# Kernel optimization log

Hardware: AMD Instinct MI355X
Metric: run time of the kernel (lower is better)

The kernel has to match this reference:

```python
import jax, jax.numpy as jnp
import numpy as np

N_NODES = 50000
N_EDGES = 800000
IN_DIM = 128
HID = 64
HEADS = 4
EMB = 128
N_GRAPHS = 64
NEG_SLOPE = 0.2


def setup_inputs() -> dict:
    key = jax.random.key(0)
    ks = jax.random.split(key, 12)
    x = jax.random.normal(ks[0], (N_NODES, IN_DIM), dtype=jnp.float32)
    edge_index = jax.random.randint(ks[1], (2, N_EDGES), 0, N_NODES, dtype=jnp.int64)
    edge_weight = jax.random.uniform(ks[2], (N_EDGES,), dtype=jnp.float32)
    batch_vec = jnp.sort(jax.random.randint(ks[3], (N_NODES,), 0, N_GRAPHS, dtype=jnp.int64))
    # GATConv layer 1: in_dim -> hid, heads=4, concat
    s1 = 1.0 / np.sqrt(IN_DIM)
    W1 = jax.random.uniform(ks[4], (IN_DIM, HEADS * HID), jnp.float32, -s1, s1)
    a_src1 = jax.random.uniform(ks[5], (HEADS, HID), jnp.float32, -s1, s1)
    a_dst1 = jax.random.uniform(ks[6], (HEADS, HID), jnp.float32, -s1, s1)
    b1 = jnp.zeros((HEADS * HID,), jnp.float32)
    # GATConv layer 2: heads*hid -> emb, heads=1, mean
    s2 = 1.0 / np.sqrt(HEADS * HID)
    W2 = jax.random.uniform(ks[7], (HEADS * HID, EMB), jnp.float32, -s2, s2)
    a_src2 = jax.random.uniform(ks[8], (1, EMB), jnp.float32, -s2, s2)
    a_dst2 = jax.random.uniform(ks[9], (1, EMB), jnp.float32, -s2, s2)
    b2 = jnp.zeros((EMB,), jnp.float32)
    return {"x": x, "edge_index": edge_index, "edge_weight": edge_weight,
            "batch_vec": batch_vec, "W1": W1, "a_src1": a_src1, "a_dst1": a_dst1,
            "b1": b1, "W2": W2, "a_src2": a_src2, "a_dst2": a_dst2, "b2": b2}


def gat_conv(x, src, dst, W, a_src, a_dst, bias, heads, out_dim, concat):
    N = x.shape[0]
    h = (x @ W).reshape(N, heads, out_dim)                 # [N,H,C]
    alpha_s = jnp.sum(h * a_src, axis=-1)                  # [N,H]
    alpha_d = jnp.sum(h * a_dst, axis=-1)                  # [N,H]
    e = jax.nn.leaky_relu(alpha_s[src] + alpha_d[dst], NEG_SLOPE)  # [E,H]
    # segment softmax over edges grouped by destination node
    m = jax.ops.segment_max(e, dst, num_segments=N)        # [N,H]
    w = jnp.exp(e - m[dst])
    z = jax.ops.segment_sum(w, dst, num_segments=N)
    alpha = w / z[dst]                                     # [E,H]
    msg = h[src] * alpha[:, :, None]                       # [E,H,C]
    out = jax.ops.segment_sum(msg, dst, num_segments=N)    # [N,H,C]
    out = out.reshape(N, heads * out_dim) if concat else out.mean(axis=1)
    return out + bias


def reference(x, edge_index, edge_weight, batch_vec, W1, a_src1, a_dst1, b1, W2, a_src2, a_dst2, b2):
    N = x.shape[0]
    loop = jnp.arange(N, dtype=edge_index.dtype)
    src = jnp.concatenate([edge_index[0], loop])           # add_self_loops=True
    dst = jnp.concatenate([edge_index[1], loop])
    h = gat_conv(x, src, dst, W1, a_src1, a_dst1, b1, HEADS, HID, True)
    h = jax.nn.elu(h)                                      # dropout = identity (eval mode)
    h = gat_conv(h, src, dst, W2, a_src2, a_dst2, b2, 1, EMB, False)
    h = jax.nn.elu(h)
    # global mean pool over batch_vec
    sums = jax.ops.segment_sum(h, batch_vec, num_segments=N_GRAPHS)
    cnts = jax.ops.segment_sum(jnp.ones((N,), h.dtype), batch_vec, num_segments=N_GRAPHS)
    return sums / jnp.maximum(cnts, 1.0)[:, None]
```

## Files before the change

kernel.cpp:

```cpp
#include <hip/hip_runtime.h>
#include <hip/hip_bf16.h>
#include <cstddef>

constexpr int N_NODES = 50000;
constexpr int N_EDGES = 800000;
constexpr int IN_DIM  = 128;
constexpr int HID     = 64;
constexpr int HEADS   = 4;
constexpr int F1      = HEADS * HID;
constexpr int EMB     = 128;
constexpr int N_GRAPHS = 64;

constexpr int DEG_BLOCKS   = (N_EDGES + 255) / 256;
constexpr int SCAN_BLOCKS  = (N_NODES + 255) / 256;
constexpr int XCONV_BLOCKS = (N_NODES * IN_DIM / 4) / 256;
constexpr int W1_FRAG = 4 * 4 * 64 * 8;
constexpr int LDSB = 264;
constexpr int AXS  = HEADS * IN_DIM + 8;
constexpr int NBUCK    = (N_NODES + 255) / 256;
constexpr int P1_CHUNK = 8192;
constexpr int P1_BLOCKS = (N_EDGES + P1_CHUNK - 1) / P1_CHUNK;
constexpr int AS_BLOCKS = N_NODES / 16;
constexpr int AGG12_BLOCKS = N_NODES / 16;
static_assert(N_NODES % 16 == 0, "16-row tiling assumes exact fit");

typedef __bf16 bf16x8 __attribute__((ext_vector_type(8)));
typedef __bf16 bf16x2 __attribute__((ext_vector_type(2)));
typedef float  f32x4  __attribute__((ext_vector_type(4)));

__device__ __forceinline__ float lrelu(float x) { return x > 0.f ? x : 0.2f * x; }
__device__ __forceinline__ float eluf(float x)  { return x > 0.f ? x : expm1f(x); }

__device__ __forceinline__ void pack_frag(const float* __restrict__ B,
                                          __bf16* __restrict__ hi,
                                          __bf16* __restrict__ lo,
                                          int pblk, int NT, int KK, int ld, int col0) {
    const int gid = pblk * 256 + threadIdx.x;
    if (gid >= NT * KK * 64) return;
    const int lane = gid & 63;
    const int rem  = gid >> 6;
    const int kk   = rem % KK;
    const int t    = rem / KK;
    const int n    = col0 + t * 16 + (lane & 15);
    const int k0   = kk * 32 + (lane >> 4) * 8;
#pragma unroll
    for (int j = 0; j < 8; j++) {
        const float v = B[(size_t)(k0 + j) * ld + n];
        const __bf16 h = (__bf16)v;
        hi[(size_t)gid * 8 + j] = h;
        lo[(size_t)gid * 8 + j] = (__bf16)(v - (float)h);
    }
}

__global__ __launch_bounds__(256) void prep_kernel(const int* __restrict__ ei,
                                                   int* __restrict__ deg,
                                                   const float* __restrict__ W1,
                                                   __bf16* __restrict__ B1h,
                                                   __bf16* __restrict__ B1l,
                                                   const float* __restrict__ W2,
                                                   __bf16* __restrict__ B2h,
                                                   __bf16* __restrict__ B2l,
                                                   const float* __restrict__ as1v,
                                                   const float* __restrict__ ad1v,
                                                   float* __restrict__ wst,
                                                   const float* __restrict__ x,
                                                   __bf16* __restrict__ xb) {
    const int b = blockIdx.x;
    if (b < DEG_BLOCKS) {
        const int e = b * 256 + threadIdx.x;
        if (e < N_EDGES) atomicAdd(&deg[ei[N_EDGES + e]], 1);
        return;
    }
    const int pb = b - DEG_BLOCKS;
    if (pb < 16) {
        const int head = pb >> 2;
        pack_frag(W1, B1h + head * W1_FRAG, B1l + head * W1_FRAG,
                  pb & 3, 4, 4, F1, head * HID);
        return;
    }
    if (pb < 32) {
        pack_frag(W2, B2h, B2l, pb - 16, 8, 8, EMB, 0);
        return;
    }
    if (pb < 36) {
        const int gid = (pb - 32) * 256 + threadIdx.x;
        const int o = gid >> 7, c = gid & 127;
        const int h = o & 3;
        const float* av = (o < 4) ? as1v : ad1v;
        float s = 0.f;
#pragma unroll 8
        for (int k = 0; k < HID; k++)
            s += W1[(size_t)c * F1 + h * HID + k] * av[h * HID + k];
        wst[o * IN_DIM + c] = s;
        return;
    }
    const int i = (pb - 36) * 256 + threadIdx.x;
    const float4 v = *(const float4*)&x[(size_t)i * 4];
    __bf16 o[4] = {(__bf16)v.x, (__bf16)v.y, (__bf16)v.z, (__bf16)v.w};
    *(ulong1*)&xb[(size_t)i * 4] = *(ulong1*)o;
}

__global__ __launch_bounds__(256) void scanA_kernel(const int* __restrict__ deg,
                                                    int* __restrict__ off,
                                                    int* __restrict__ partial, int N) {
    __shared__ int sm[256];
    const int t = threadIdx.x;
    const int i = blockIdx.x * 256 + t;
    const int v = (i < N) ? deg[i] : 0;
    sm[t] = v;
    __syncthreads();
    int val = v;
#pragma unroll
    for (int o = 1; o < 256; o <<= 1) {
        const int add = (t >= o) ? sm[t - o] : 0;
        __syncthreads();
        val += add;
        sm[t] = val;
        __syncthreads();
    }
    if (i < N) off[i] = val - v;
    if (t == 255) partial[blockIdx.x] = val;
}

__global__ __launch_bounds__(256) void scanB_kernel(int* __restrict__ partial,
                                                    int* __restrict__ off_last) {
    __shared__ int sm[256];
    const int t = threadIdx.x;
    const int v = (t < SCAN_BLOCKS) ? partial[t] : 0;
    sm[t] = v;
    __syncthreads();
    int val = v;
#pragma unroll
    for (int o = 1; o < 256; o <<= 1) {
        const int add = (t >= o) ? sm[t - o] : 0;
        __syncthreads();
        val += add;
        sm[t] = val;
        __syncthreads();
    }
    if (t < SCAN_BLOCKS) partial[t] = val - v;
    if (t == SCAN_BLOCKS - 1) *off_last = val;
}

__global__ __launch_bounds__(256) void scanC_kernel(int* __restrict__ off,
                                                    const int* __restrict__ partial,
                                                    int* __restrict__ cur,
                                                    int* __restrict__ gcur, int N) {
    const int i = blockIdx.x * 256 + threadIdx.x;
    if (i < N) {
        const int o = off[i] + partial[blockIdx.x];
        off[i] = o;
        cur[i] = 0;
        if ((i & 255) == 0) gcur[i >> 8] = o;
    }
}

__global__ __launch_bounds__(256) void as_scatter_kernel(
        const float* __restrict__ x, const float* __restrict__ wst,
        float* __restrict__ as_out, float* __restrict__ ad_out,
        const int* __restrict__ ei, int* __restrict__ gcur,
        unsigned* __restrict__ stage) {
    const int tid = threadIdx.x;
    if (blockIdx.x < AS_BLOCKS) {
        const int n   = blockIdx.x * 16 + (tid >> 4);
        const int l16 = tid & 15;
        const int d8  = l16 * 8;
        const float4 xa = *(const float4*)&x[(size_t)n * IN_DIM + d8];
        const float4 xc = *(const float4*)&x[(size_t)n * IN_DIM + d8 + 4];
        float p[8];
#pragma unroll
        for (int o = 0; o < 8; o++) {
            const float4 wa = *(const float4*)&wst[o * IN_DIM + d8];
            const float4 wb = *(const float4*)&wst[o * IN_DIM + d8 + 4];
            p[o] = xa.x * wa.x + xa.y * wa.y + xa.z * wa.z + xa.w * wa.w
                 + xc.x * wb.x + xc.y * wb.y + xc.z * wb.z + xc.w * wb.w;
        }
#pragma unroll
        for (int off = 1; off < 16; off <<= 1) {
#pragma unroll
            for (int o = 0; o < 8; o++) p[o] += __shfl_xor(p[o], off);
        }
        if (l16 == 0) {
            *(float4*)&as_out[n * HEADS] = (float4){p[0], p[1], p[2], p[3]};
            *(float4*)&ad_out[n * HEADS] = (float4){p[4], p[5], p[6], p[7]};
        }
        return;
    }
    __shared__ int lhist[NBUCK];
    __shared__ int lbase[NBUCK];
    const int e0 = (blockIdx.x - AS_BLOCKS) * P1_CHUNK;
    for (int b = tid; b < NBUCK; b += 256) lhist[b] = 0;
    __syncthreads();
    for (int i = 0; i < P1_CHUNK / 256; i++) {
        const int e = e0 + i * 256 + tid;
        if (e < N_EDGES) atomicAdd(&lhist[ei[N_EDGES + e] >> 8], 1);
    }
    __syncthreads();
    for (int b = tid; b < NBUCK; b += 256) {
        const int c = lhist[b];
        lbase[b] = c ? atomicAdd(&gcur[b], c) : 0;
    }
    __syncthreads();
    for (int b = tid; b < NBUCK; b += 256) lhist[b] = 0;
    __syncthreads();
    for (int i = 0; i < P1_CHUNK / 256; i++) {
        const int e = e0 + i * 256 + tid;
        if (e < N_EDGES) {
            const int s = ei[e], d = ei[N_EDGES + e];
            const int bk = d >> 8;
            const int r  = atomicAdd(&lhist[bk], 1);
            stage[lbase[bk] + r] = (unsigned)s | ((unsigned)d << 16);
        }
    }
}

__global__ __launch_bounds__(256) void w1s_kernel(const unsigned* __restrict__ stage,
                                                  const int* __restrict__ off,
                                                  int* __restrict__ cur,
                                                  const float* __restrict__ as1,
                                                  const float* __restrict__ ad1,
                                                  int* __restrict__ col,
                                                  float4* __restrict__ w4, int E) {
    const int i = blockIdx.x * 256 + threadIdx.x;
    if (i >= E) return;
    const unsigned p = stage[i];
    const int s = (int)(p & 0xFFFFu);
    const int d = (int)(p >> 16);
    const float4 a = *(const float4*)&as1[s * HEADS];
    const float4 b = *(const float4*)&ad1[d * HEADS];
    const int pos = off[d] + atomicAdd(&cur[d], 1);
    float4 o;
    o.x = __expf(lrelu(a.x + b.x));
    o.y = __expf(lrelu(a.y + b.y));
    o.z = __expf(lrelu(a.z + b.z));
    o.w = __expf(lrelu(a.w + b.w));
    col[pos] = s;
    w4[pos] = o;
}

__global__ __launch_bounds__(256, 4) void agg_gemm12_kernel(
        const int* __restrict__ off, const int* __restrict__ col,
        const float4* __restrict__ w4, const __bf16* __restrict__ xb,
        const float* __restrict__ as1, const float* __restrict__ ad1,
        const __bf16* __restrict__ B1h, const __bf16* __restrict__ B1l,
        const float* __restrict__ b1,
        const __bf16* __restrict__ B2h, const __bf16* __restrict__ B2l,
        const float* __restrict__ avs, const float* __restrict__ avd,
        __bf16* __restrict__ g2b, float* __restrict__ as_out,
        float* __restrict__ ad_out, int M) {
    __shared__ __bf16 axh[16 * AXS];
    __shared__ __bf16 axl[16 * AXS];
    __shared__ float pps[4][16], pdd[4][16];
    __bf16* const smh = axh;
    __bf16* const sml = axl;
    const int tid  = threadIdx.x;
    const int wave = tid >> 6, lane = tid & 63;
    const int quad = lane >> 4, l16 = lane & 15;
    const int row0 = blockIdx.x * 16;

    {
        const int ln = wave * 4 + quad;
        const int w  = row0 + ln;
        const int d8 = l16 * 8;
        float acc[HEADS][8];
        float z[HEADS];
        {
            const float4 asv = *(const float4*)&as1[w * HEADS];
            const float4 adv = *(const float4*)&ad1[w * HEADS];
            const float ws0 = __expf(lrelu(asv.x + adv.x));
            const float ws1 = __expf(lrelu(asv.y + adv.y));
            const float ws2 = __expf(lrelu(asv.z + adv.z));
            const float ws3 = __expf(lrelu(asv.w + adv.w));
            const bf16x8 xv = *(const bf16x8*)&xb[(size_t)w * IN_DIM + d8];
#pragma unroll
            for (int d = 0; d < 8; d++) {
                const float xf = (float)xv[d];
                acc[0][d] = ws0 * xf; acc[1][d] = ws1 * xf;
                acc[2][d] = ws2 * xf; acc[3][d] = ws3 * xf;
            }
            z[0] = ws0; z[1] = ws1; z[2] = ws2; z[3] = ws3;
        }
        const int jb = off[w], je = off[w + 1];
        int j = jb;
        for (; j + 3 < je; j += 4) {
            int    s[4];
            float4 ww[4];
            bf16x8 bv[4];
#pragma unroll
            for (int u = 0; u < 4; u++) s[u] = col[j + u];
#pragma unroll
            for (int u = 0; u < 4; u++) ww[u] = w4[j + u];
#pragma unroll
            for (int u = 0; u < 4; u++)
                bv[u] = *(const bf16x8*)&xb[(size_t)s[u] * IN_DIM + d8];
#pragma unroll
            for (int u = 0; u < 4; u++) {
#pragma unroll
                for (int d = 0; d < 8; d++) {
                    const float xf = (float)bv[u][d];
                    acc[0][d] += ww[u].x * xf;
                    acc[1][d] += ww[u].y * xf;
                    acc[2][d] += ww[u].z * xf;
                    acc[3][d] += ww[u].w * xf;
                }
                z[0] += ww[u].x; z[1] += ww[u].y;
                z[2] += ww[u].z; z[3] += ww[u].w;
            }
        }
        for (; j < je; j++) {
            const int s0 = col[j];
            const float4 w0 = w4[j];
            const bf16x8 b0 = *(const bf16x8*)&xb[(size_t)s0 * IN_DIM + d8];
#pragma unroll
            for (int d = 0; d < 8; d++) {
                const float xf = (float)b0[d];
                acc[0][d] += w0.x * xf; acc[1][d] += w0.y * xf;
                acc[2][d] += w0.z * xf; acc[3][d] += w0.w * xf;
            }
            z[0] += w0.x; z[1] += w0.y; z[2] += w0.z; z[3] += w0.w;
        }
#pragma unroll
        for (int h = 0; h < HEADS; h++) {
            const float inv = 1.f / z[h];
            bf16x8 hv, lv;
#pragma unroll
            for (int d = 0; d < 8; d++) {
                const float v = acc[h][d] * inv;
                const __bf16 hh = (__bf16)v;
                hv[d] = hh;
                lv[d] = (__bf16)(v - (float)hh);
            }
            const int o = ln * AXS + h * IN_DIM + d8;
            *(bf16x8*)&axh[o] = hv;
            *(bf16x8*)&axl[o] = lv;
        }
    }
    __syncthreads();

    {
        bf16x8 ahv[4], alv[4];
        const int abase = l16 * AXS + wave * IN_DIM;
#pragma unroll
        for (int kk = 0; kk < 4; kk++) {
            const int k0 = kk * 32 + quad * 8;
            ahv[kk] = *(const bf16x8*)&axh[abase + k0];
            alv[kk] = *(const bf16x8*)&axl[abase + k0];
        }
        __syncthreads();

        f32x4 acc1[4];
#pragma unroll
        for (int t = 0; t < 4; t++) acc1[t] = (f32x4){0.f, 0.f, 0.f, 0.f};
#pragma unroll
        for (int kk = 0; kk < 4; kk++) {
#pragma unroll
            for (int t = 0; t < 4; t++) {
                const size_t bi = (size_t)wave * W1_FRAG +
                                  ((size_t)(t * 4 + kk) * 64 + lane) * 8;
                bf16x8 bhv = *(const bf16x8*)&B1h[bi];
                bf16x8 blv = *(const bf16x8*)&B1l[bi];
                acc1[t] = __builtin_amdgcn_mfma_f32_16x16x32_bf16(ahv[kk], bhv, acc1[t], 0, 0, 0);
                acc1[t] = __builtin_amdgcn_mfma_f32_16x16x32_bf16(alv[kk], bhv, acc1[t], 0, 0, 0);
                acc1[t] = __builtin_amdgcn_mfma_f32_16x16x32_bf16(ahv[kk], blv, acc1[t], 0, 0, 0);
            }
        }
#pragma unroll
        for (int t = 0; t < 4; t++) {
            const int c = wave * 64 + t * 16 + l16;
            const float bb = b1[c];
#pragma unroll
            for (int r = 0; r < 4; r++) {
                const float v = eluf(acc1[t][r] + bb);
                const __bf16 hh = (__bf16)v;
                smh[(quad * 4 + r) * LDSB + c] = hh;
                sml[(quad * 4 + r) * LDSB + c] = (__bf16)(v - (float)hh);
            }
        }
    }
    __syncthreads();

    f32x4 acc2[2];
#pragma unroll
    for (int t = 0; t < 2; t++) acc2[t] = (f32x4){0.f, 0.f, 0.f, 0.f};
    const int arow = l16 * LDSB;
#pragma unroll
    for (int kk = 0; kk < 8; kk++) {
        const int k0 = kk * 32 + quad * 8;
        bf16x8 ah = *(const bf16x8*)&smh[arow + k0];
        bf16x8 al = *(const bf16x8*)&sml[arow + k0];
#pragma unroll
        for (int tt = 0; tt < 2; tt++) {
            const int t = wave * 2 + tt;
            const size_t bi = ((size_t)(t * 8 + kk) * 64 + lane) * 8;
            bf16x8 bhv = *(const bf16x8*)&B2h[bi];
            bf16x8 blv = *(const bf16x8*)&B2l[bi];
            acc2[tt] = __builtin_amdgcn_mfma_f32_16x16x32_bf16(ah, bhv, acc2[tt], 0, 0, 0);
            acc2[tt] = __builtin_amdgcn_mfma_f32_16x16x32_bf16(al, bhv, acc2[tt], 0, 0, 0);
            acc2[tt] = __builtin_amdgcn_mfma_f32_16x16x32_bf16(ah, blv, acc2[tt], 0, 0, 0);
        }
    }

    const int rowS = row0 + quad * 4;
#pragma unroll
    for (int tt = 0; tt < 2; tt++) {
        const int t = wave * 2 + tt;
#pragma unroll
        for (int r = 0; r < 4; r++) {
            const int rr = rowS + r;
            if (rr < M) g2b[(size_t)rr * EMB + t * 16 + l16] = (__bf16)acc2[tt][r];
        }
    }
#pragma unroll
    for (int r = 0; r < 4; r++) {
        float ps = 0.f, pd = 0.f;
#pragma unroll
        for (int tt = 0; tt < 2; tt++) {
            const int c = (wave * 2 + tt) * 16 + l16;
            ps += acc2[tt][r] * avs[c];
            pd += acc2[tt][r] * avd[c];
        }
#pragma unroll
        for (int o = 1; o < 16; o <<= 1) {
            ps += __shfl_xor(ps, o);
            pd += __shfl_xor(pd, o);
        }
        if (l16 == 0) {
            pps[wave][quad * 4 + r] = ps;
            pdd[wave][quad * 4 + r] = pd;
        }
    }
    __syncthreads();
    if (tid < 16) {
        const int rr = row0 + tid;
        if (rr < M) {
            as_out[rr] = pps[0][tid] + pps[1][tid] + pps[2][tid] + pps[3][tid];
            ad_out[rr] = pdd[0][tid] + pdd[1][tid] + pdd[2][tid] + pdd[3][tid];
        }
    }
}

__global__ __launch_bounds__(256) void agg2_kernel(const int* __restrict__ off,
                                                   const int* __restrict__ col,
                                                   const float* __restrict__ as2,
                                                   const float* __restrict__ ad2,
                                                   const __bf16* __restrict__ g2b,
                                                   float* __restrict__ out2, int N) {
    const int w  = blockIdx.x * 16 + (threadIdx.x >> 4);
    const int d8 = (threadIdx.x & 15) * 8;
    const float ad2w = ad2[w];
    float acc[8];
    float z;
    {
        const float wt = __expf(lrelu(as2[w] + ad2w));
        const bf16x8 hv = *(const bf16x8*)&g2b[(size_t)w * EMB + d8];
#pragma unroll
        for (int d = 0; d < 8; d++) acc[d] = wt * (float)hv[d];
        z = wt;
    }
    const int jb = off[w], je = off[w + 1];
    int j = jb;
    for (; j + 3 < je; j += 4) {
        int s[4];
#pragma unroll
        for (int u = 0; u < 4; u++) s[u] = col[j + u];
        float av[4];
#pragma unroll
        for (int u = 0; u < 4; u++) av[u] = as2[s[u]];
        bf16x8 bv[4];
#pragma unroll
        for (int u = 0; u < 4; u++)
            bv[u] = *(const bf16x8*)&g2b[(size_t)s[u] * EMB + d8];
#pragma unroll
        for (int u = 0; u < 4; u++) {
            const float wt = __expf(lrelu(av[u] + ad2w));
#pragma unroll
            for (int d = 0; d < 8; d++) acc[d] += wt * (float)bv[u][d];
            z += wt;
        }
    }
    for (; j < je; j++) {
        const int s0 = col[j];
        const float wt = __expf(lrelu(as2[s0] + ad2w));
        const bf16x8 b0 = *(const bf16x8*)&g2b[(size_t)s0 * EMB + d8];
#pragma unroll
        for (int d = 0; d < 8; d++) acc[d] += wt * (float)b0[d];
        z += wt;
    }
    const float inv = 1.f / z;
    float4 o0, o1;
    o0.x = acc[0] * inv; o0.y = acc[1] * inv; o0.z = acc[2] * inv; o0.w = acc[3] * inv;
    o1.x = acc[4] * inv; o1.y = acc[5] * inv; o1.z = acc[6] * inv; o1.w = acc[7] * inv;
    *(float4*)&out2[(size_t)w * EMB + d8]     = o0;
    *(float4*)&out2[(size_t)w * EMB + d8 + 4] = o1;
}

__global__ __launch_bounds__(128) void pool_kernel(const float* __restrict__ out2,
                                                   const float* __restrict__ b2,
                                                   const int* __restrict__ batch,
                                                   float* __restrict__ pool,
                                                   float* __restrict__ cnt, int N) {
    const int c = threadIdx.x;
    const int n0 = blockIdx.x * 64;
    const int nend = min(n0 + 64, N);
    const float bias = b2[c];
    float acc = 0.f, cacc = 0.f;
    int curg = batch[n0];
    for (int n = n0; n < nend; n++) {
        const int g = batch[n];
        if (g != curg) {
            atomicAdd(&pool[curg * EMB + c], acc);
            if (c == 0) atomicAdd(&cnt[curg], cacc);
            acc = 0.f; cacc = 0.f; curg = g;
        }
        float v = out2[(size_t)n * EMB + c] + bias;
        v = v > 0.f ? v : expm1f(v);
        acc += v;
        cacc += 1.f;
    }
    atomicAdd(&pool[curg * EMB + c], acc);
    if (c == 0) atomicAdd(&cnt[curg], cacc);
}

__global__ __launch_bounds__(256) void div_kernel(const float* __restrict__ pool,
                                                  const float* __restrict__ cnt,
                                                  float* __restrict__ out) {
    const int i = blockIdx.x * 256 + threadIdx.x;
    out[i] = pool[i] / fmaxf(cnt[i >> 7], 1.f);
}

extern "C" void kernel_launch(void* const* d_in, const int* in_sizes, int n_in,
                              void* d_out, int out_size, void* d_ws, size_t ws_size,
                              hipStream_t stream) {
    const float* x      = (const float*)d_in[0];
    const int*   ei     = (const int*)d_in[1];
    const int*   batch  = (const int*)d_in[3];
    const float* W1     = (const float*)d_in[4];
    const float* a_src1 = (const float*)d_in[5];
    const float* a_dst1 = (const float*)d_in[6];
    const float* b1     = (const float*)d_in[7];
    const float* W2     = (const float*)d_in[8];
    const float* a_src2 = (const float*)d_in[9];
    const float* a_dst2 = (const float*)d_in[10];
    const float* b2     = (const float*)d_in[11];
    float* out = (float*)d_out;

    const int N = N_NODES, E = N_EDGES;

    size_t cur_off = 0;
    auto carve = [&](size_t bytes) {
        size_t o = cur_off;
        cur_off = (cur_off + bytes + 255) & ~(size_t)255;
        return (char*)d_ws + o;
    };
    int* deg     = (int*)carve((size_t)N * 4);
    float* pool  = (float*)carve((size_t)N_GRAPHS * EMB * 4);
    float* cnt   = (float*)carve((size_t)N_GRAPHS * 4);
    const size_t zero_bytes = cur_off;
    int* curp    = (int*)carve((size_t)N * 4);
    int* partial = (int*)carve((size_t)SCAN_BLOCKS * 4);
    int* gcur    = (int*)carve((size_t)NBUCK * 4);
    unsigned* stage = (unsigned*)carve((size_t)E * 4);
    float* wst   = (float*)carve((size_t)8 * IN_DIM * 4);
    __bf16* B1h  = (__bf16*)carve((size_t)HEADS * W1_FRAG * 2);
    __bf16* B1l  = (__bf16*)carve((size_t)HEADS * W1_FRAG * 2);
    __bf16* B2h  = (__bf16*)carve((size_t)F1 * EMB * 2);
    __bf16* B2l  = (__bf16*)carve((size_t)F1 * EMB * 2);
    __bf16* xb   = (__bf16*)carve((size_t)N * IN_DIM * 2);
    int* off     = (int*)carve((size_t)(N + 1) * 4);
    int* col     = (int*)carve((size_t)E * 4);
    float4* w4   = (float4*)carve((size_t)E * 16);
    __bf16* g2b  = (__bf16*)carve((size_t)N * EMB * 2);
    float* out2  = (float*)carve((size_t)N * EMB * 4);
    float* as1   = (float*)carve((size_t)N * HEADS * 4);
    float* ad1   = (float*)carve((size_t)N * HEADS * 4);
    float* as2   = (float*)carve((size_t)N * 4);
    float* ad2   = (float*)carve((size_t)N * 4);

    hipMemsetAsync(d_ws, 0, zero_bytes, stream);

    prep_kernel<<<DEG_BLOCKS + 36 + XCONV_BLOCKS, 256, 0, stream>>>(
        ei, deg, W1, B1h, B1l, W2, B2h, B2l, a_src1, a_dst1, wst, x, xb);

    scanA_kernel<<<SCAN_BLOCKS, 256, 0, stream>>>(deg, off, partial, N);
    scanB_kernel<<<1, 256, 0, stream>>>(partial, &off[N]);
    scanC_kernel<<<SCAN_BLOCKS, 256, 0, stream>>>(off, partial, curp, gcur, N);

    as_scatter_kernel<<<AS_BLOCKS + P1_BLOCKS, 256, 0, stream>>>(
        x, wst, as1, ad1, ei, gcur, stage);

    w1s_kernel<<<DEG_BLOCKS, 256, 0, stream>>>(stage, off, curp, as1, ad1, col, w4, E);

    agg_gemm12_kernel<<<AGG12_BLOCKS, 256, 0, stream>>>(off, col, w4, xb, as1, ad1,
                                                        B1h, B1l, b1, B2h, B2l,
                                                        a_src2, a_dst2,
                                                        g2b, as2, ad2, N);

    agg2_kernel<<<AGG12_BLOCKS, 256, 0, stream>>>(off, col, as2, ad2, g2b, out2, N);

    pool_kernel<<<(N + 63) / 64, 128, 0, stream>>>(out2, b2, batch, pool, cnt, N);
    div_kernel<<<(N_GRAPHS * EMB) / 256, 256, 0, stream>>>(pool, cnt, out);
}
```

Baseline: 329.3 us.

## Fuse pooling into agg2, fold bf16 cast of x into alpha kernel, pack FMAs

The bias, ELU and global mean-pool step moves into the layer-2 aggregation kernel. Each wave reduces its rows across lanes when all four of its nodes share a graph, then issues atomics, so the out2 buffer and the pool_kernel launch go away. The x-to-bf16 conversion now happens in as_scatter_kernel, which already reads x, so x is not read a second time. The aggregation loops use f32x2 vectors so the compiler can emit packed FMAs. In exchange, pool atomics are now spread across more blocks, which can cause more contention than the old per-64-node batching.

```diff
diff --git a/kernel.cpp b/kernel.cpp
--- a/kernel.cpp
+++ b/kernel.cpp
@@ -13,7 +13,6 @@
 
 constexpr int DEG_BLOCKS   = (N_EDGES + 255) / 256;
 constexpr int SCAN_BLOCKS  = (N_NODES + 255) / 256;
-constexpr int XCONV_BLOCKS = (N_NODES * IN_DIM / 4) / 256;
 constexpr int W1_FRAG = 4 * 4 * 64 * 8;
 constexpr int LDSB = 264;
 constexpr int AXS  = HEADS * IN_DIM + 8;
@@ -27,9 +26,11 @@
 typedef __bf16 bf16x8 __attribute__((ext_vector_type(8)));
 typedef __bf16 bf16x2 __attribute__((ext_vector_type(2)));
 typedef float  f32x4  __attribute__((ext_vector_type(4)));
+typedef float  f32x2  __attribute__((ext_vector_type(2)));
 
 __device__ __forceinline__ float lrelu(float x) { return x > 0.f ? x : 0.2f * x; }
 __device__ __forceinline__ float eluf(float x)  { return x > 0.f ? x : expm1f(x); }
+__device__ __forceinline__ f32x2 s2(float s)    { return (f32x2){s, s}; }
 
 __device__ __forceinline__ void pack_frag(const float* __restrict__ B,
                                           __bf16* __restrict__ hi,
@@ -62,9 +63,7 @@
                                                    __bf16* __restrict__ B2l,
                                                    const float* __restrict__ as1v,
                                                    const float* __restrict__ ad1v,
-                                                   float* __restrict__ wst,
-                                                   const float* __restrict__ x,
-                                                   __bf16* __restrict__ xb) {
+                                                   float* __restrict__ wst) {
     const int b = blockIdx.x;
     if (b < DEG_BLOCKS) {
         const int e = b * 256 + threadIdx.x;
@@ -82,22 +81,15 @@
         pack_frag(W2, B2h, B2l, pb - 16, 8, 8, EMB, 0);
         return;
     }
-    if (pb < 36) {
-        const int gid = (pb - 32) * 256 + threadIdx.x;
-        const int o = gid >> 7, c = gid & 127;
-        const int h = o & 3;
-        const float* av = (o < 4) ? as1v : ad1v;
-        float s = 0.f;
+    const int gid = (pb - 32) * 256 + threadIdx.x;
+    const int o = gid >> 7, c = gid & 127;
+    const int h = o & 3;
+    const float* av = (o < 4) ? as1v : ad1v;
+    float s = 0.f;
 #pragma unroll 8
-        for (int k = 0; k < HID; k++)
-            s += W1[(size_t)c * F1 + h * HID + k] * av[h * HID + k];
-        wst[o * IN_DIM + c] = s;
-        return;
-    }
-    const int i = (pb - 36) * 256 + threadIdx.x;
-    const float4 v = *(const float4*)&x[(size_t)i * 4];
-    __bf16 o[4] = {(__bf16)v.x, (__bf16)v.y, (__bf16)v.z, (__bf16)v.w};
-    *(ulong1*)&xb[(size_t)i * 4] = *(ulong1*)o;
+    for (int k = 0; k < HID; k++)
+        s += W1[(size_t)c * F1 + h * HID + k] * av[h * HID + k];
+    wst[o * IN_DIM + c] = s;
 }
 
 __global__ __launch_bounds__(256) void scanA_kernel(const int* __restrict__ deg,
@@ -158,6 +150,7 @@
 __global__ __launch_bounds__(256) void as_scatter_kernel(
         const float* __restrict__ x, const float* __restrict__ wst,
         float* __restrict__ as_out, float* __restrict__ ad_out,
+        __bf16* __restrict__ xb,
         const int* __restrict__ ei, int* __restrict__ gcur,
         unsigned* __restrict__ stage) {
     const int tid = threadIdx.x;
@@ -167,6 +160,12 @@
         const int d8  = l16 * 8;
         const float4 xa = *(const float4*)&x[(size_t)n * IN_DIM + d8];
         const float4 xc = *(const float4*)&x[(size_t)n * IN_DIM + d8 + 4];
+        bf16x8 bw;
+        bw[0] = (__bf16)xa.x; bw[1] = (__bf16)xa.y;
+        bw[2] = (__bf16)xa.z; bw[3] = (__bf16)xa.w;
+        bw[4] = (__bf16)xc.x; bw[5] = (__bf16)xc.y;
+        bw[6] = (__bf16)xc.z; bw[7] = (__bf16)xc.w;
+        *(bf16x8*)&xb[(size_t)n * IN_DIM + d8] = bw;
         float p[8];
 #pragma unroll
         for (int o = 0; o < 8; o++) {
@@ -262,7 +261,7 @@
         const int ln = wave * 4 + quad;
         const int w  = row0 + ln;
         const int d8 = l16 * 8;
-        float acc[HEADS][8];
+        f32x2 acc[HEADS][4];
         float z[HEADS];
         {
             const float4 asv = *(const float4*)&as1[w * HEADS];
@@ -273,10 +272,12 @@
             const float ws3 = __expf(lrelu(asv.w + adv.w));
             const bf16x8 xv = *(const bf16x8*)&xb[(size_t)w * IN_DIM + d8];
 #pragma unroll
-            for (int d = 0; d < 8; d++) {
-                const float xf = (float)xv[d];
-                acc[0][d] = ws0 * xf; acc[1][d] = ws1 * xf;
-                acc[2][d] = ws2 * xf; acc[3][d] = ws3 * xf;
+            for (int p = 0; p < 4; p++) {
+                const f32x2 xf = {(float)xv[2 * p], (float)xv[2 * p + 1]};
+                acc[0][p] = s2(ws0) * xf;
+                acc[1][p] = s2(ws1) * xf;
+                acc[2][p] = s2(ws2) * xf;
+                acc[3][p] = s2(ws3) * xf;
             }
             z[0] = ws0; z[1] = ws1; z[2] = ws2; z[3] = ws3;
         }
@@ -295,13 +296,16 @@
                 bv[u] = *(const bf16x8*)&xb[(size_t)s[u] * IN_DIM + d8];
 #pragma unroll
             for (int u = 0; u < 4; u++) {
-#pragma unroll
-                for (int d = 0; d < 8; d++) {
-                    const float xf = (float)bv[u][d];
-                    acc[0][d] += ww[u].x * xf;
-                    acc[1][d] += ww[u].y * xf;
-                    acc[2][d] += ww[u].z * xf;
-                    acc[3][d] += ww[u].w * xf;
+                f32x2 xf[4];
+#pragma unroll
+                for (int p = 0; p < 4; p++)
+                    xf[p] = (f32x2){(float)bv[u][2 * p], (float)bv[u][2 * p + 1]};
+#pragma unroll
+                for (int p = 0; p < 4; p++) {
+                    acc[0][p] += s2(ww[u].x) * xf[p];
+                    acc[1][p] += s2(ww[u].y) * xf[p];
+                    acc[2][p] += s2(ww[u].z) * xf[p];
+                    acc[3][p] += s2(ww[u].w) * xf[p];
                 }
                 z[0] += ww[u].x; z[1] += ww[u].y;
                 z[2] += ww[u].z; z[3] += ww[u].w;
@@ -312,10 +316,12 @@
             const float4 w0 = w4[j];
             const bf16x8 b0 = *(const bf16x8*)&xb[(size_t)s0 * IN_DIM + d8];
 #pragma unroll
-            for (int d = 0; d < 8; d++) {
-                const float xf = (float)b0[d];
-                acc[0][d] += w0.x * xf; acc[1][d] += w0.y * xf;
-                acc[2][d] += w0.z * xf; acc[3][d] += w0.w * xf;
+            for (int p = 0; p < 4; p++) {
+                const f32x2 xf = {(float)b0[2 * p], (float)b0[2 * p + 1]};
+                acc[0][p] += s2(w0.x) * xf;
+                acc[1][p] += s2(w0.y) * xf;
+                acc[2][p] += s2(w0.z) * xf;
+                acc[3][p] += s2(w0.w) * xf;
             }
             z[0] += w0.x; z[1] += w0.y; z[2] += w0.z; z[3] += w0.w;
         }
@@ -324,11 +330,13 @@
             const float inv = 1.f / z[h];
             bf16x8 hv, lv;
 #pragma unroll
-            for (int d = 0; d < 8; d++) {
-                const float v = acc[h][d] * inv;
-                const __bf16 hh = (__bf16)v;
-                hv[d] = hh;
-                lv[d] = (__bf16)(v - (float)hh);
+            for (int p = 0; p < 4; p++) {
+                const f32x2 vv = acc[h][p] * s2(inv);
+                const __bf16 h0 = (__bf16)vv[0], h1 = (__bf16)vv[1];
+                hv[2 * p]     = h0;
+                hv[2 * p + 1] = h1;
+                lv[2 * p]     = (__bf16)(vv[0] - (float)h0);
+                lv[2 * p + 1] = (__bf16)(vv[1] - (float)h1);
             }
             const int o = ln * AXS + h * IN_DIM + d8;
             *(bf16x8*)&axh[o] = hv;
@@ -444,17 +452,24 @@
                                                    const float* __restrict__ as2,
                                                    const float* __restrict__ ad2,
                                                    const __bf16* __restrict__ g2b,
-                                                   float* __restrict__ out2, int N) {
+                                                   const int* __restrict__ batch,
+                                                   const float* __restrict__ b2,
+                                                   float* __restrict__ pool,
+                                                   float* __restrict__ cnt, int N) {
     const int w  = blockIdx.x * 16 + (threadIdx.x >> 4);
-    const int d8 = (threadIdx.x & 15) * 8;
+    const int l16 = threadIdx.x & 15;
+    const int d8 = l16 * 8;
     const float ad2w = ad2[w];
-    float acc[8];
+    f32x2 acc[4];
     float z;
     {
         const float wt = __expf(lrelu(as2[w] + ad2w));
         const bf16x8 hv = *(const bf16x8*)&g2b[(size_t)w * EMB + d8];
 #pragma unroll
-        for (int d = 0; d < 8; d++) acc[d] = wt * (float)hv[d];
+        for (int p = 0; p < 4; p++) {
+            const f32x2 xf = {(float)hv[2 * p], (float)hv[2 * p + 1]};
+            acc[p] = s2(wt) * xf;
+        }
         z = wt;
     }
     const int jb = off[w], je = off[w + 1];
@@ -474,7 +489,10 @@
         for (int u = 0; u < 4; u++) {
             const float wt = __expf(lrelu(av[u] + ad2w));
 #pragma unroll
-            for (int d = 0; d < 8; d++) acc[d] += wt * (float)bv[u][d];
+            for (int p = 0; p < 4; p++) {
+                const f32x2 xf = {(float)bv[u][2 * p], (float)bv[u][2 * p + 1]};
+                acc[p] += s2(wt) * xf;
+            }
             z += wt;
         }
     }
@@ -483,42 +501,46 @@
         const float wt = __expf(lrelu(as2[s0] + ad2w));
         const bf16x8 b0 = *(const bf16x8*)&g2b[(size_t)s0 * EMB + d8];
 #pragma unroll
-        for (int d = 0; d < 8; d++) acc[d] += wt * (float)b0[d];
+        for (int p = 0; p < 4; p++) {
+            const f32x2 xf = {(float)b0[2 * p], (float)b0[2 * p + 1]};
+            acc[p] += s2(wt) * xf;
+        }
         z += wt;
     }
     const float inv = 1.f / z;
-    float4 o0, o1;
-    o0.x = acc[0] * inv; o0.y = acc[1] * inv; o0.z = acc[2] * inv; o0.w = acc[3] * inv;
-    o1.x = acc[4] * inv; o1.y = acc[5] * inv; o1.z = acc[6] * inv; o1.w = acc[7] * inv;
-    *(float4*)&out2[(size_t)w * EMB + d8]     = o0;
-    *(float4*)&out2[(size_t)w * EMB + d8 + 4] = o1;
-}
-
-__global__ __launch_bounds__(128) void pool_kernel(const float* __restrict__ out2,
-                                                   const float* __restrict__ b2,
-                                                   const int* __restrict__ batch,
-                                                   float* __restrict__ pool,
-                                                   float* __restrict__ cnt, int N) {
-    const int c = threadIdx.x;
-    const int n0 = blockIdx.x * 64;
-    const int nend = min(n0 + 64, N);
-    const float bias = b2[c];
-    float acc = 0.f, cacc = 0.f;
-    int curg = batch[n0];
-    for (int n = n0; n < nend; n++) {
-        const int g = batch[n];
-        if (g != curg) {
-            atomicAdd(&pool[curg * EMB + c], acc);
-            if (c == 0) atomicAdd(&cnt[curg], cacc);
-            acc = 0.f; cacc = 0.f; curg = g;
-        }
-        float v = out2[(size_t)n * EMB + c] + bias;
-        v = v > 0.f ? v : expm1f(v);
-        acc += v;
-        cacc += 1.f;
-    }
-    atomicAdd(&pool[curg * EMB + c], acc);
-    if (c == 0) atomicAdd(&cnt[curg], cacc);
+    const float4 bb0 = *(const float4*)&b2[d8];
+    const float4 bb1 = *(const float4*)&b2[d8 + 4];
+    float v[8];
+    {
+        const f32x2 t0 = acc[0] * s2(inv), t1 = acc[1] * s2(inv);
+        const f32x2 t2 = acc[2] * s2(inv), t3 = acc[3] * s2(inv);
+        v[0] = eluf(t0[0] + bb0.x); v[1] = eluf(t0[1] + bb0.y);
+        v[2] = eluf(t1[0] + bb0.z); v[3] = eluf(t1[1] + bb0.w);
+        v[4] = eluf(t2[0] + bb1.x); v[5] = eluf(t2[1] + bb1.y);
+        v[6] = eluf(t3[0] + bb1.z); v[7] = eluf(t3[1] + bb1.w);
+    }
+    const int g = batch[w];
+    const int gx = __shfl_xor(g, 16);
+    const int gy = __shfl_xor(g, 32);
+    const bool uni = __all(g == gx && g == gy);
+    if (uni) {
+#pragma unroll
+        for (int d = 0; d < 8; d++) {
+            v[d] += __shfl_xor(v[d], 16);
+            v[d] += __shfl_xor(v[d], 32);
+        }
+        if ((threadIdx.x & 63) < 16) {
+#pragma unroll
+            for (int d = 0; d < 8; d++)
+                atomicAdd(&pool[g * EMB + d8 + d], v[d]);
+            if (l16 == 0) atomicAdd(&cnt[g], 4.f);
+        }
+    } else {
+#pragma unroll
+        for (int d = 0; d < 8; d++)
+            atomicAdd(&pool[g * EMB + d8 + d], v[d]);
+        if (l16 == 0) atomicAdd(&cnt[g], 1.f);
+    }
 }
 
 __global__ __launch_bounds__(256) void div_kernel(const float* __restrict__ pool,
@@ -570,7 +592,6 @@
     int* col     = (int*)carve((size_t)E * 4);
     float4* w4   = (float4*)carve((size_t)E * 16);
     __bf16* g2b  = (__bf16*)carve((size_t)N * EMB * 2);
-    float* out2  = (float*)carve((size_t)N * EMB * 4);
     float* as1   = (float*)carve((size_t)N * HEADS * 4);
     float* ad1   = (float*)carve((size_t)N * HEADS * 4);
     float* as2   = (float*)carve((size_t)N * 4);
@@ -578,15 +599,15 @@
 
     hipMemsetAsync(d_ws, 0, zero_bytes, stream);
 
-    prep_kernel<<<DEG_BLOCKS + 36 + XCONV_BLOCKS, 256, 0, stream>>>(
-        ei, deg, W1, B1h, B1l, W2, B2h, B2l, a_src1, a_dst1, wst, x, xb);
+    prep_kernel<<<DEG_BLOCKS + 36, 256, 0, stream>>>(
+        ei, deg, W1, B1h, B1l, W2, B2h, B2l, a_src1, a_dst1, wst);
 
     scanA_kernel<<<SCAN_BLOCKS, 256, 0, stream>>>(deg, off, partial, N);
     scanB_kernel<<<1, 256, 0, stream>>>(partial, &off[N]);
     scanC_kernel<<<SCAN_BLOCKS, 256, 0, stream>>>(off, partial, curp, gcur, N);
 
     as_scatter_kernel<<<AS_BLOCKS + P1_BLOCKS, 256, 0, stream>>>(
-        x, wst, as1, ad1, ei, gcur, stage);
+        x, wst, as1, ad1, xb, ei, gcur, stage);
 
     w1s_kernel<<<DEG_BLOCKS, 256, 0, stream>>>(stage, off, curp, as1, ad1, col, w4, E);
 
@@ -595,8 +616,8 @@
                                                         a_src2, a_dst2,
                                                         g2b, as2, ad2, N);
 
-    agg2_kernel<<<AGG12_BLOCKS, 256, 0, stream>>>(off, col, as2, ad2, g2b, out2, N);
-
-    pool_kernel<<<(N + 63) / 64, 128, 0, stream>>>(out2, b2, batch, pool, cnt, N);
+    agg2_kernel<<<AGG12_BLOCKS, 256, 0, stream>>>(off, col, as2, ad2, g2b,
+                                                  batch, b2, pool, cnt, N);
+
     div_kernel<<<(N_GRAPHS * EMB) / 256, 256, 0, stream>>>(pool, cnt, out);
 }
```

Measured after the change: 415.2 us. 1.26x slower.
